# Kernel optimization log

Measured on AMD Instinct MI355X. Metric: run time of the kernel, lower is better.

Reference implementation:

```python
import jax, jax.numpy as jnp
import numpy as np

N_NODES = 100000
N_EDGES = 1600000
IN_FEATS = 128
N_HIDDEN = 128
N_CLASSES = 64


def _degree_norms(src, dst, n_nodes):
    ones = jnp.ones(src.shape[0], dtype=jnp.float32)
    deg_out = jax.ops.segment_sum(ones, src, num_segments=n_nodes)  # out-degree of src nodes
    deg_in = jax.ops.segment_sum(ones, dst, num_segments=n_nodes)   # in-degree of dst nodes
    norm_src = jax.lax.rsqrt(jnp.clip(deg_out, 1.0))  # D_src^{-1/2}, clamp like DGL
    norm_dst = jax.lax.rsqrt(jnp.clip(deg_in, 1.0))   # D_dst^{-1/2}
    return norm_src, norm_dst


def _graph_conv(x, src, dst, norm_src, norm_dst, W, b, relu):
    # DGL GraphConv, norm='both': D_dst^{-1/2} A D_src^{-1/2} X W + b
    h = x * norm_src[:, None]
    agg = jax.ops.segment_sum(h[src], dst, num_segments=x.shape[0])  # [N, d]
    h = agg * norm_dst[:, None]
    h = h @ W + b
    return jax.nn.relu(h) if relu else h


def setup_inputs() -> dict:
    key = jax.random.key(0)
    ks = jax.random.split(key, 10)
    features = jax.random.normal(ks[0], (N_NODES, IN_FEATS), dtype=jnp.float32)
    src = jax.random.randint(ks[1], (N_EDGES,), 0, N_NODES, dtype=jnp.int64 if jax.config.read('jax_enable_x64') else jnp.int32)
    dst = jax.random.randint(ks[2], (N_EDGES,), 0, N_NODES, dtype=src.dtype)
    s = 1.0 / np.sqrt(IN_FEATS)
    W0 = jax.random.uniform(ks[3], (IN_FEATS, N_HIDDEN), jnp.float32, -s, s)
    b0 = jnp.zeros((N_HIDDEN,), jnp.float32)
    sh = 1.0 / np.sqrt(N_HIDDEN)
    W1 = jax.random.uniform(ks[4], (N_HIDDEN, N_HIDDEN), jnp.float32, -sh, sh)
    b1 = jnp.zeros((N_HIDDEN,), jnp.float32)
    W2 = jax.random.uniform(ks[5], (N_HIDDEN, N_CLASSES), jnp.float32, -sh, sh)
    b2 = jnp.zeros((N_CLASSES,), jnp.float32)
    return {"features": features, "src": src, "dst": dst,
            "W0": W0, "b0": b0, "W1": W1, "b1": b1, "W2": W2, "b2": b2}


def reference(features, src, dst, W0, b0, W1, b1, W2, b2):
    norm_src, norm_dst = _degree_norms(src, dst, features.shape[0])
    # dropout is identity in eval mode
    h = _graph_conv(features, src, dst, norm_src, norm_dst, W0, b0, relu=True)
    h = _graph_conv(h, src, dst, norm_src, norm_dst, W1, b1, relu=True)
    h = _graph_conv(h, src, dst, norm_src, norm_dst, W2, b2, relu=False)
    return h
```

## Files before the change

kernel.cpp:

```cpp
#include <hip/hip_runtime.h>
#include <hip/hip_fp16.h>

#define K_FEATS 128
#define RBSHIFT 9
#define RB 512

typedef short bf16x8 __attribute__((ext_vector_type(8)));
typedef float f32x4 __attribute__((ext_vector_type(4)));

__device__ __forceinline__ unsigned short bf16_rne(float x) {
    unsigned u = __float_as_uint(x);
    unsigned r = (u + 0x7FFFu + ((u >> 16) & 1u)) >> 16;
    return (unsigned short)r;
}
__device__ __forceinline__ float bf16_f(unsigned short h) {
    return __uint_as_float(((unsigned)h) << 16);
}

__global__ __launch_bounds__(256) void count_split(
    const int* __restrict__ src, const int* __restrict__ dst,
    int* __restrict__ partialS, int* __restrict__ partialD,
    const float* __restrict__ W0, const float* __restrict__ W1,
    const float* __restrict__ W2,
    unsigned short* __restrict__ W0th, unsigned short* __restrict__ W0tl,
    unsigned short* __restrict__ W1th, unsigned short* __restrict__ W1tl,
    unsigned short* __restrict__ W2th, unsigned short* __restrict__ W2tl,
    int ne, int chunkA, int C, int NB)
{
    __shared__ int hS[256];
    __shared__ int hD[256];
    int bid = blockIdx.x, t = threadIdx.x;
    if (bid < C) {
        if (t < NB) { hS[t] = 0; hD[t] = 0; }
        __syncthreads();
        int e0 = bid * chunkA, e1 = min(ne, e0 + chunkA);
        for (int e = e0 + t; e < e1; e += 256) {
            atomicAdd(&hS[src[e] >> RBSHIFT], 1);
            atomicAdd(&hD[dst[e] >> RBSHIFT], 1);
        }
        __syncthreads();
        for (int i = t; i < NB; i += 256) {
            partialS[i * C + bid] = hS[i];
            partialD[i * C + bid] = hD[i];
        }
    } else {
        int e = (bid - C) * 256 + t;
        const float* W; unsigned short *Wh, *Wl; int NC, idx;
        bool ok = true;
        if (e < 16384)      { W = W0; Wh = W0th; Wl = W0tl; NC = 128; idx = e; }
        else if (e < 32768) { W = W1; Wh = W1th; Wl = W1tl; NC = 128; idx = e - 16384; }
        else if (e < 40960) { W = W2; Wh = W2th; Wl = W2tl; NC = 64;  idx = e - 32768; }
        else ok = false;
        if (ok) {
            int c = idx >> 7, kk = idx & 127;
            float w = W[kk * NC + c];
            unsigned short h = bf16_rne(w);
            Wh[idx] = h;
            Wl[idx] = bf16_rne(w - bf16_f(h));
        }
    }
}

__global__ __launch_bounds__(256) void bucket_prefix(
    int* __restrict__ partialS, int* __restrict__ partialD,
    int* __restrict__ totS, int* __restrict__ totD, int C, int NB)
{
    __shared__ int sh[256];
    int b = blockIdx.x, t = threadIdx.x;
    int* part = blockIdx.y ? partialD : partialS;
    int* tot = blockIdx.y ? totD : totS;
    int v = (t < C) ? part[b * C + t] : 0;
    sh[t] = v;
    __syncthreads();
    for (int off = 1; off < 256; off <<= 1) {
        int x = (t >= off) ? sh[t - off] : 0;
        __syncthreads();
        sh[t] += x;
        __syncthreads();
    }
    if (t < C) part[b * C + t] = sh[t] - v;
    if (t == 255) tot[b] = sh[255];
}

__global__ __launch_bounds__(256) void bucket_scatter(
    const int* __restrict__ src, const int* __restrict__ dst,
    const int* __restrict__ partialS, const int* __restrict__ partialD,
    const int* __restrict__ totS, const int* __restrict__ totD,
    unsigned short* __restrict__ src_bkt, int* __restrict__ edge_bkt,
    int ne, int chunkA, int C, int NB)
{
    __shared__ int shB[256];
    __shared__ int curS[256];
    __shared__ int curD[256];
    int bid = blockIdx.x, t = threadIdx.x;
    int vS = (t < NB) ? totS[t] : 0;
    shB[t] = vS;
    __syncthreads();
    for (int off = 1; off < 256; off <<= 1) {
        int x = (t >= off) ? shB[t - off] : 0;
        __syncthreads();
        shB[t] += x;
        __syncthreads();
    }
    if (t < NB) curS[t] = (shB[t] - vS) + partialS[t * C + bid];
    __syncthreads();
    int vD = (t < NB) ? totD[t] : 0;
    shB[t] = vD;
    __syncthreads();
    for (int off = 1; off < 256; off <<= 1) {
        int x = (t >= off) ? shB[t - off] : 0;
        __syncthreads();
        shB[t] += x;
        __syncthreads();
    }
    if (t < NB) curD[t] = (shB[t] - vD) + partialD[t * C + bid];
    __syncthreads();
    int e0 = bid * chunkA, e1 = min(ne, e0 + chunkA);
    for (int e = e0 + t; e < e1; e += 256) {
        int s = src[e];
        int d = dst[e];
        int posD = atomicAdd(&curD[d >> RBSHIFT], 1);
        edge_bkt[posD] = ((d & (RB - 1)) << 17) | s;
        int posS = atomicAdd(&curS[s >> RBSHIFT], 1);
        src_bkt[posS] = (unsigned short)(s & (RB - 1));
    }
}

__global__ __launch_bounds__(256) void fine_all(
    const int* __restrict__ edge_bkt, const unsigned short* __restrict__ src_bkt,
    const int* __restrict__ totS, const int* __restrict__ totD,
    int* __restrict__ row_off, float* __restrict__ norm_dst,
    float* __restrict__ norm_src, int* __restrict__ csr, int n, int ne, int NB)
{
    __shared__ int shA[RB];
    __shared__ int shB[256];
    int bid = blockIdx.x, t = threadIdx.x;
    int y = bid & 1, b = bid >> 1;
    const int* tot = y ? totS : totD;
    int v = (t < NB) ? tot[t] : 0;
    shB[t] = v;
    __syncthreads();
    for (int off = 1; off < 256; off <<= 1) {
        int x = (t >= off) ? shB[t - off] : 0;
        __syncthreads();
        shB[t] += x;
        __syncthreads();
    }
    int e1 = shB[b];
    int ebase = e1 - tot[b];
    __syncthreads();
    int lo = b << RBSHIFT;
    for (int i = t; i < RB; i += 256) shA[i] = 0;
    __syncthreads();
    if (y == 1) {
        for (int e = ebase + t; e < e1; e += 256)
            atomicAdd(&shA[src_bkt[e]], 1);
        __syncthreads();
        for (int i = t; i < RB; i += 256) {
            int g = lo + i;
            if (g < n) norm_src[g] = rsqrtf((float)max(shA[i], 1));
        }
        return;
    }
    if (bid == 0 && t == 0) row_off[n] = ne;
    for (int e = ebase + t; e < e1; e += 256)
        atomicAdd(&shA[(unsigned)edge_bkt[e] >> 17], 1);
    __syncthreads();
    int v0 = shA[2 * t], v1 = shA[2 * t + 1];
    shB[t] = v0 + v1;
    __syncthreads();
    for (int off = 1; off < 256; off <<= 1) {
        int x = (t >= off) ? shB[t - off] : 0;
        __syncthreads();
        shB[t] += x;
        __syncthreads();
    }
    int excl = shB[t] - (v0 + v1) + ebase;
    int g0 = lo + 2 * t, g1 = g0 + 1;
    if (g0 < n) { row_off[g0] = excl;      norm_dst[g0] = rsqrtf((float)max(v0, 1)); }
    if (g1 < n) { row_off[g1] = excl + v0; norm_dst[g1] = rsqrtf((float)max(v1, 1)); }
    shA[2 * t] = excl;
    shA[2 * t + 1] = excl + v0;
    __syncthreads();
    for (int e = ebase + t; e < e1; e += 256) {
        int p = edge_bkt[e];
        int pos = atomicAdd(&shA[(unsigned)p >> 17], 1);
        csr[pos] = p & 0x1FFFF;
    }
}

template <int NCOL, bool HALF_OUT, int MODE>
__global__ __launch_bounds__(256) void gemm_mfma(
    const __half* __restrict__ X16, const float* __restrict__ Xf,
    const unsigned short* __restrict__ Wth, const unsigned short* __restrict__ Wtl,
    const float* __restrict__ scale, void* __restrict__ outv, int n)
{
    constexpr int CT = NCOL / 16;
    constexpr int CHUNKS = NCOL * 16;
    __shared__ unsigned short Ws[16 * NCOL * 8];

    int t = threadIdx.x;
    int w = t >> 6, lane = t & 63, m = lane & 15, q = lane >> 4;
    int r0 = blockIdx.x * 128 + w * 32;

    f32x4 acc[2][CT];
#pragma unroll
    for (int i = 0; i < 2; i++)
#pragma unroll
        for (int j = 0; j < CT; j++) acc[i][j] = (f32x4){0.f, 0.f, 0.f, 0.f};

    bf16x8 ah[2][4], al[2][4];
#pragma unroll
    for (int rt = 0; rt < 2; rt++) {
        int row = r0 + rt * 16 + m;
        size_t base = (size_t)row * K_FEATS + q * 8;
#pragma unroll
        for (int k = 0; k < 4; k++) {
            float f[8];
            if (MODE == 0) {
                if (row < n) {
                    *(float4*)&f[0] = *(const float4*)(Xf + base + k * 32);
                    *(float4*)&f[4] = *(const float4*)(Xf + base + k * 32 + 4);
                } else {
#pragma unroll
                    for (int j = 0; j < 8; j++) f[j] = 0.f;
                }
            } else {
                union { uint4 q4; __half h[8]; } U;
                U.q4 = *(const uint4*)(X16 + base + k * 32);
#pragma unroll
                for (int j = 0; j < 8; j++) f[j] = __half2float(U.h[j]);
            }
            union { bf16x8 v; unsigned short u[8]; } H, L;
#pragma unroll
            for (int j = 0; j < 8; j++) {
                H.u[j] = bf16_rne(f[j]);
                L.u[j] = bf16_rne(f[j] - bf16_f(H.u[j]));
            }
            ah[rt][k] = H.v;
            al[rt][k] = L.v;
        }
    }

#pragma unroll
    for (int i = 0; i < CHUNKS / 256; i++) {
        int g = t + i * 256;
        int col = g >> 4, sec = g & 15;
        *(bf16x8*)(Ws + sec * NCOL * 8 + ((col ^ (sec & 7)) * 8)) =
            *(const bf16x8*)(Wth + g * 8);
    }
    __syncthreads();
#pragma unroll
    for (int k = 0; k < 4; k++) {
        int sec = k * 4 + q;
#pragma unroll
        for (int ct = 0; ct < CT; ct++) {
            bf16x8 bh = *(const bf16x8*)(Ws + sec * NCOL * 8 +
                                         (((ct * 16 + m) ^ (sec & 7)) * 8));
            acc[0][ct] = __builtin_amdgcn_mfma_f32_16x16x32_bf16(ah[0][k], bh, acc[0][ct], 0, 0, 0);
            acc[0][ct] = __builtin_amdgcn_mfma_f32_16x16x32_bf16(al[0][k], bh, acc[0][ct], 0, 0, 0);
            acc[1][ct] = __builtin_amdgcn_mfma_f32_16x16x32_bf16(ah[1][k], bh, acc[1][ct], 0, 0, 0);
            acc[1][ct] = __builtin_amdgcn_mfma_f32_16x16x32_bf16(al[1][k], bh, acc[1][ct], 0, 0, 0);
        }
    }
    __syncthreads();
#pragma unroll
    for (int i = 0; i < CHUNKS / 256; i++) {
        int g = t + i * 256;
        int col = g >> 4, sec = g & 15;
        *(bf16x8*)(Ws + sec * NCOL * 8 + ((col ^ (sec & 7)) * 8)) =
            *(const bf16x8*)(Wtl + g * 8);
    }
    __syncthreads();
#pragma unroll
    for (int k = 0; k < 4; k++) {
        int sec = k * 4 + q;
#pragma unroll
        for (int ct = 0; ct < CT; ct++) {
            bf16x8 bl = *(const bf16x8*)(Ws + sec * NCOL * 8 +
                                         (((ct * 16 + m) ^ (sec & 7)) * 8));
            acc[0][ct] = __builtin_amdgcn_mfma_f32_16x16x32_bf16(ah[0][k], bl, acc[0][ct], 0, 0, 0);
            acc[1][ct] = __builtin_amdgcn_mfma_f32_16x16x32_bf16(ah[1][k], bl, acc[1][ct], 0, 0, 0);
        }
    }

#pragma unroll
    for (int rt = 0; rt < 2; rt++) {
        int rb = r0 + rt * 16 + q * 4;
#pragma unroll
        for (int reg = 0; reg < 4; reg++) {
            int row = rb + reg;
            if (row < n) {
                float s = scale[row];
#pragma unroll
                for (int ct = 0; ct < CT; ct++) {
                    float v = acc[rt][ct][reg] * s;
                    size_t o = (size_t)row * NCOL + ct * 16 + m;
                    if (HALF_OUT) ((__half*)outv)[o] = __float2half(v);
                    else ((float*)outv)[o] = v;
                }
            }
        }
    }
}

template <bool RELU>
__global__ __launch_bounds__(256) void aggregate4h(
    const __half* __restrict__ Tm, const int* __restrict__ row_off,
    const int* __restrict__ csr, const float* __restrict__ ndst,
    const float* __restrict__ bias, __half* __restrict__ Oh, int n)
{
    int lane = threadIdx.x & 15;
    int team = threadIdx.x >> 4;
    int fb = lane * 8;
    float b[8];
    *(float4*)&b[0] = *(const float4*)(bias + fb);
    *(float4*)&b[4] = *(const float4*)(bias + fb + 4);
    int stride = gridDim.x * 16;
    for (int v = blockIdx.x * 16 + team; v < n; v += stride) {
        int s = row_off[v], e = row_off[v + 1];
        float nd = ndst[v];
        float a[8] = {};
        int i = s;
        for (; i + 4 <= e; i += 4) {
            int u0 = csr[i], u1 = csr[i + 1], u2 = csr[i + 2], u3 = csr[i + 3];
            union { uint4 q; __half h[8]; } U0, U1, U2, U3;
            U0.q = *(const uint4*)(Tm + (size_t)u0 * 128 + fb);
            U1.q = *(const uint4*)(Tm + (size_t)u1 * 128 + fb);
            U2.q = *(const uint4*)(Tm + (size_t)u2 * 128 + fb);
            U3.q = *(const uint4*)(Tm + (size_t)u3 * 128 + fb);
#pragma unroll
            for (int j = 0; j < 8; j++)
                a[j] += (__half2float(U0.h[j]) + __half2float(U1.h[j])) +
                        (__half2float(U2.h[j]) + __half2float(U3.h[j]));
        }
        for (; i < e; i++) {
            int u = csr[i];
            union { uint4 q; __half h[8]; } U;
            U.q = *(const uint4*)(Tm + (size_t)u * 128 + fb);
#pragma unroll
            for (int j = 0; j < 8; j++) a[j] += __half2float(U.h[j]);
        }
        union { uint4 q; __half h[8]; } O;
#pragma unroll
        for (int j = 0; j < 8; j++) {
            float o = nd * a[j] + b[j];
            if (RELU) o = fmaxf(o, 0.f);
            O.h[j] = __float2half(o);
        }
        *(uint4*)(Oh + (size_t)v * 128 + fb) = O.q;
    }
}

__global__ __launch_bounds__(256) void aggregate2h(
    const __half* __restrict__ Tm, const int* __restrict__ row_off,
    const int* __restrict__ csr, const float* __restrict__ ndst,
    const float* __restrict__ bias, float* __restrict__ out, int n)
{
    int lane = threadIdx.x & 7;
    int team = threadIdx.x >> 3;
    int fb = lane * 8;
    float b[8];
    *(float4*)&b[0] = *(const float4*)(bias + fb);
    *(float4*)&b[4] = *(const float4*)(bias + fb + 4);
    int stride = gridDim.x * 32;
    for (int v = blockIdx.x * 32 + team; v < n; v += stride) {
        int s = row_off[v], e = row_off[v + 1];
        float nd = ndst[v];
        float a[8] = {};
        int i = s;
        for (; i + 4 <= e; i += 4) {
            int u0 = csr[i], u1 = csr[i + 1], u2 = csr[i + 2], u3 = csr[i + 3];
            union { uint4 q; __half h[8]; } U0, U1, U2, U3;
            U0.q = *(const uint4*)(Tm + (size_t)u0 * 64 + fb);
            U1.q = *(const uint4*)(Tm + (size_t)u1 * 64 + fb);
            U2.q = *(const uint4*)(Tm + (size_t)u2 * 64 + fb);
            U3.q = *(const uint4*)(Tm + (size_t)u3 * 64 + fb);
#pragma unroll
            for (int j = 0; j < 8; j++)
                a[j] += (__half2float(U0.h[j]) + __half2float(U1.h[j])) +
                        (__half2float(U2.h[j]) + __half2float(U3.h[j]));
        }
        for (; i < e; i++) {
            int u = csr[i];
            union { uint4 q; __half h[8]; } U;
            U.q = *(const uint4*)(Tm + (size_t)u * 64 + fb);
#pragma unroll
            for (int j = 0; j < 8; j++) a[j] += __half2float(U.h[j]);
        }
        float o[8];
#pragma unroll
        for (int j = 0; j < 8; j++) o[j] = nd * a[j] + b[j];
        *(float4*)(out + (size_t)v * 64 + fb) = *(float4*)&o[0];
        *(float4*)(out + (size_t)v * 64 + fb + 4) = *(float4*)&o[4];
    }
}

extern "C" void kernel_launch(void* const* d_in, const int* in_sizes, int n_in,
                              void* d_out, int out_size, void* d_ws, size_t ws_size,
                              hipStream_t stream)
{
    const float* features = (const float*)d_in[0];
    const int* src = (const int*)d_in[1];
    const int* dst = (const int*)d_in[2];
    const float* W0 = (const float*)d_in[3];
    const float* b0 = (const float*)d_in[4];
    const float* W1 = (const float*)d_in[5];
    const float* b1 = (const float*)d_in[6];
    const float* W2 = (const float*)d_in[7];
    const float* b2 = (const float*)d_in[8];

    int n = in_sizes[0] / K_FEATS;
    int ne = in_sizes[1];
    int n_pad = (n + 127) & ~127;

    char* ws = (char*)d_ws;
    size_t off = 0;
    auto take = [&](size_t bytes) -> char* {
        char* p = ws + off;
        off = (off + bytes + 255) & ~(size_t)255;
        return p;
    };
    __half* Xbuf = (__half*)take((size_t)n_pad * 128 * 2);
    __half* Th = (__half*)take((size_t)n_pad * 128 * 2);
    int* csr = (int*)take((size_t)ne * 4);
    int* edge_bkt = (int*)take((size_t)ne * 4);
    unsigned short* src_bkt = (unsigned short*)take((size_t)ne * 2);
    int* row_off = (int*)take((size_t)(n + 1) * 4);
    float* norm_src = (float*)take((size_t)n * 4);
    float* norm_dst = (float*)take((size_t)n * 4);
    unsigned short* W0th = (unsigned short*)take(128 * 128 * 2);
    unsigned short* W0tl = (unsigned short*)take(128 * 128 * 2);
    unsigned short* W1th = (unsigned short*)take(128 * 128 * 2);
    unsigned short* W1tl = (unsigned short*)take(128 * 128 * 2);
    unsigned short* W2th = (unsigned short*)take(64 * 128 * 2);
    unsigned short* W2tl = (unsigned short*)take(64 * 128 * 2);

    int NB = (n + RB - 1) >> RBSHIFT;
    int chunkA = 8192;
    int C = (ne + chunkA - 1) / chunkA;
    if (C > 256) { chunkA = (ne + 255) / 256; C = (ne + chunkA - 1) / chunkA; }

    int* partialS = (int*)take((size_t)NB * C * 4);
    int* partialD = (int*)take((size_t)NB * C * 4);
    int* totS = (int*)take((size_t)NB * 4);
    int* totD = (int*)take((size_t)NB * 4);

    count_split<<<C + 160, 256, 0, stream>>>(
        src, dst, partialS, partialD,
        W0, W1, W2, W0th, W0tl, W1th, W1tl, W2th, W2tl,
        ne, chunkA, C, NB);
    bucket_prefix<<<dim3(NB, 2), 256, 0, stream>>>(partialS, partialD, totS, totD, C, NB);
    bucket_scatter<<<C, 256, 0, stream>>>(src, dst, partialS, partialD,
                                          totS, totD, src_bkt, edge_bkt,
                                          ne, chunkA, C, NB);
    fine_all<<<2 * NB, 256, 0, stream>>>(edge_bkt, src_bkt, totS, totD,
                                         row_off, norm_dst, norm_src, csr,
                                         n, ne, NB);

    int gblocks = n_pad / 128;
    int ablocks4 = (n + 15) / 16;
    int ablocks2 = (n + 31) / 32;

    gemm_mfma<128, true, 0><<<gblocks, 256, 0, stream>>>(
        nullptr, features, W0th, W0tl, norm_src, Th, n);
    aggregate4h<true><<<ablocks4, 256, 0, stream>>>(Th, row_off, csr, norm_dst, b0,
                                                    Xbuf, n);
    gemm_mfma<128, true, 1><<<gblocks, 256, 0, stream>>>(
        Xbuf, nullptr, W1th, W1tl, norm_src, Th, n);
    aggregate4h<true><<<ablocks4, 256, 0, stream>>>(Th, row_off, csr, norm_dst, b1,
                                                    Xbuf, n);
    gemm_mfma<64, true, 1><<<gblocks, 256, 0, stream>>>(
        Xbuf, nullptr, W2th, W2tl, norm_src, Th, n);
    aggregate2h<<<ablocks2, 256, 0, stream>>>(Th, row_off, csr, norm_dst, b2,
                                              (float*)d_out, n);
}
```

Baseline: 377.7 us.

## Store aggregated activations as bf16 hi/lo pairs and split aggregation launches

The hidden-layer aggregation now writes its output directly as a pair of bf16 arrays (high and residual low parts), and the next GEMM loads these pre-split operands instead of converting fp16 to fp32 and splitting into bf16 pairs itself. Each aggregation is also split into two launches over the two halves of the node range. This moves the split arithmetic out of the GEMM's load path, but doubles the activation bytes written by aggregation and read by the GEMM. It also adds an extra kernel launch per layer.

```diff
diff --git a/kernel.cpp b/kernel.cpp
--- a/kernel.cpp
+++ b/kernel.cpp
@@ -192,6 +192,7 @@
 template <int NCOL, bool HALF_OUT, int MODE>
 __global__ __launch_bounds__(256) void gemm_mfma(
     const __half* __restrict__ X16, const float* __restrict__ Xf,
+    const unsigned short* __restrict__ XH, const unsigned short* __restrict__ XL,
     const unsigned short* __restrict__ Wth, const unsigned short* __restrict__ Wtl,
     const float* __restrict__ scale, void* __restrict__ outv, int n)
 {
@@ -216,29 +217,34 @@
         size_t base = (size_t)row * K_FEATS + q * 8;
 #pragma unroll
         for (int k = 0; k < 4; k++) {
-            float f[8];
-            if (MODE == 0) {
-                if (row < n) {
-                    *(float4*)&f[0] = *(const float4*)(Xf + base + k * 32);
-                    *(float4*)&f[4] = *(const float4*)(Xf + base + k * 32 + 4);
+            if (MODE == 2) {
+                ah[rt][k] = *(const bf16x8*)(XH + base + k * 32);
+                al[rt][k] = *(const bf16x8*)(XL + base + k * 32);
+            } else {
+                float f[8];
+                if (MODE == 0) {
+                    if (row < n) {
+                        *(float4*)&f[0] = *(const float4*)(Xf + base + k * 32);
+                        *(float4*)&f[4] = *(const float4*)(Xf + base + k * 32 + 4);
+                    } else {
+#pragma unroll
+                        for (int j = 0; j < 8; j++) f[j] = 0.f;
+                    }
                 } else {
-#pragma unroll
-                    for (int j = 0; j < 8; j++) f[j] = 0.f;
+                    union { uint4 q4; __half h[8]; } U;
+                    U.q4 = *(const uint4*)(X16 + base + k * 32);
+#pragma unroll
+                    for (int j = 0; j < 8; j++) f[j] = __half2float(U.h[j]);
                 }
-            } else {
-                union { uint4 q4; __half h[8]; } U;
-                U.q4 = *(const uint4*)(X16 + base + k * 32);
-#pragma unroll
-                for (int j = 0; j < 8; j++) f[j] = __half2float(U.h[j]);
+                union { bf16x8 v; unsigned short u[8]; } H, L;
+#pragma unroll
+                for (int j = 0; j < 8; j++) {
+                    H.u[j] = bf16_rne(f[j]);
+                    L.u[j] = bf16_rne(f[j] - bf16_f(H.u[j]));
+                }
+                ah[rt][k] = H.v;
+                al[rt][k] = L.v;
             }
-            union { bf16x8 v; unsigned short u[8]; } H, L;
-#pragma unroll
-            for (int j = 0; j < 8; j++) {
-                H.u[j] = bf16_rne(f[j]);
-                L.u[j] = bf16_rne(f[j] - bf16_f(H.u[j]));
-            }
-            ah[rt][k] = H.v;
-            al[rt][k] = L.v;
         }
     }
 
@@ -304,11 +310,12 @@
     }
 }
 
-template <bool RELU>
 __global__ __launch_bounds__(256) void aggregate4h(
     const __half* __restrict__ Tm, const int* __restrict__ row_off,
     const int* __restrict__ csr, const float* __restrict__ ndst,
-    const float* __restrict__ bias, __half* __restrict__ Oh, int n)
+    const float* __restrict__ bias,
+    unsigned short* __restrict__ OhH, unsigned short* __restrict__ OhL,
+    int vbase, int vend)
 {
     int lane = threadIdx.x & 15;
     int team = threadIdx.x >> 4;
@@ -317,7 +324,7 @@
     *(float4*)&b[0] = *(const float4*)(bias + fb);
     *(float4*)&b[4] = *(const float4*)(bias + fb + 4);
     int stride = gridDim.x * 16;
-    for (int v = blockIdx.x * 16 + team; v < n; v += stride) {
+    for (int v = vbase + blockIdx.x * 16 + team; v < vend; v += stride) {
         int s = row_off[v], e = row_off[v + 1];
         float nd = ndst[v];
         float a[8] = {};
@@ -341,14 +348,17 @@
 #pragma unroll
             for (int j = 0; j < 8; j++) a[j] += __half2float(U.h[j]);
         }
-        union { uint4 q; __half h[8]; } O;
+        union { uint4 q; unsigned short u[8]; } H, L;
 #pragma unroll
         for (int j = 0; j < 8; j++) {
             float o = nd * a[j] + b[j];
-            if (RELU) o = fmaxf(o, 0.f);
-            O.h[j] = __float2half(o);
-        }
-        *(uint4*)(Oh + (size_t)v * 128 + fb) = O.q;
+            o = fmaxf(o, 0.f);
+            unsigned short hh = bf16_rne(o);
+            H.u[j] = hh;
+            L.u[j] = bf16_rne(o - bf16_f(hh));
+        }
+        *(uint4*)(OhH + (size_t)v * 128 + fb) = H.q;
+        *(uint4*)(OhL + (size_t)v * 128 + fb) = L.q;
     }
 }
 
@@ -421,7 +431,8 @@
         off = (off + bytes + 255) & ~(size_t)255;
         return p;
     };
-    __half* Xbuf = (__half*)take((size_t)n_pad * 128 * 2);
+    unsigned short* XbufH = (unsigned short*)take((size_t)n_pad * 128 * 2);
+    unsigned short* XbufL = (unsigned short*)take((size_t)n_pad * 128 * 2);
     __half* Th = (__half*)take((size_t)n_pad * 128 * 2);
     int* csr = (int*)take((size_t)ne * 4);
     int* edge_bkt = (int*)take((size_t)ne * 4);
@@ -459,19 +470,23 @@
                                          n, ne, NB);
 
     int gblocks = n_pad / 128;
-    int ablocks4 = (n + 15) / 16;
-    int ablocks2 = (n + 31) / 32;
+    int half = (n + 1) / 2;
+    int ah_blocks = (half + 15) / 16;
 
     gemm_mfma<128, true, 0><<<gblocks, 256, 0, stream>>>(
-        nullptr, features, W0th, W0tl, norm_src, Th, n);
-    aggregate4h<true><<<ablocks4, 256, 0, stream>>>(Th, row_off, csr, norm_dst, b0,
-                                                    Xbuf, n);
-    gemm_mfma<128, true, 1><<<gblocks, 256, 0, stream>>>(
-        Xbuf, nullptr, W1th, W1tl, norm_src, Th, n);
-    aggregate4h<true><<<ablocks4, 256, 0, stream>>>(Th, row_off, csr, norm_dst, b1,
-                                                    Xbuf, n);
-    gemm_mfma<64, true, 1><<<gblocks, 256, 0, stream>>>(
-        Xbuf, nullptr, W2th, W2tl, norm_src, Th, n);
-    aggregate2h<<<ablocks2, 256, 0, stream>>>(Th, row_off, csr, norm_dst, b2,
-                                              (float*)d_out, n);
-}
+        nullptr, features, nullptr, nullptr, W0th, W0tl, norm_src, Th, n);
+    aggregate4h<<<ah_blocks, 256, 0, stream>>>(Th, row_off, csr, norm_dst, b0,
+                                               XbufH, XbufL, 0, half);
+    aggregate4h<<<ah_blocks, 256, 0, stream>>>(Th, row_off, csr, norm_dst, b0,
+                                               XbufH, XbufL, half, n);
+    gemm_mfma<128, true, 2><<<gblocks, 256, 0, stream>>>(
+        nullptr, nullptr, XbufH, XbufL, W1th, W1tl, norm_src, Th, n);
+    aggregate4h<<<ah_blocks, 256, 0, stream>>>(Th, row_off, csr, norm_dst, b1,
+                                               XbufH, XbufL, 0, half);
+    aggregate4h<<<ah_blocks, 256, 0, stream>>>(Th, row_off, csr, norm_dst, b1,
+                                               XbufH, XbufL, half, n);
+    gemm_mfma<64, true, 2><<<gblocks, 256, 0, stream>>>(
+        nullptr, nullptr, XbufH, XbufL, W2th, W2tl, norm_src, Th, n);
+    aggregate2h<<<(n + 31) / 32, 256, 0, stream>>>(Th, row_off, csr, norm_dst, b2,
+                                                   (float*)d_out, n);
+}
```

After: 408.5 us. +8.2%, slower.
